# Performance work log

Measured on AMD Instinct MI355X. Metric: run time of the kernel, lower is better.

## Reference

```python
import jax, jax.numpy as jnp
import numpy as np


def _normal_distance(n1, n2):
    # Cosine-style normal distance: 1 - <n1, n2>. The original module stubs
    # this as 0; we use the canonical mesh-normal loss so the cdist+argmin+
    # gather chain is exercised end-to-end.
    return 1.0 - jnp.sum(n1 * n2, axis=-1)


def setup_inputs() -> dict:
    key = jax.random.key(0)
    k1, k2, k3, k4 = jax.random.split(key, 4)
    N, M = 8192, 32768
    pred_pts = jax.random.normal(k1, (1, N, 3), dtype=jnp.float32)
    pred_nrm = jax.random.normal(k2, (1, N, 3), dtype=jnp.float32)
    gt_pts = jax.random.normal(k3, (1, M, 3), dtype=jnp.float32)
    gt_nrm = jax.random.normal(k4, (1, M, 3), dtype=jnp.float32)
    # unit normals, as on a real mesh
    pred_nrm = pred_nrm / jnp.linalg.norm(pred_nrm, axis=-1, keepdims=True)
    gt_nrm = gt_nrm / jnp.linalg.norm(gt_nrm, axis=-1, keepdims=True)
    return {
        "predicted_points_batch": pred_pts,
        "predicted_normals_batch": pred_nrm,
        "gt_points_batch": gt_pts,
        "gt_normals_batch": gt_nrm,
    }


def reference(predicted_points_batch, predicted_normals_batch,
              gt_points_batch, gt_normals_batch):
    # Original forward returns inside the first loop iteration -> element 0 only.
    p = predicted_points_batch[0]    # [N,3]
    pn = predicted_normals_batch[0]  # [N,3]
    g = gt_points_batch[0]           # [M,3]
    gn = gt_normals_batch[0]         # [M,3]

    # Squared pairwise distances (monotone in true cdist; only argmin is used).
    # d2[i,j] = |p_i|^2 + |g_j|^2 - 2 p_i . g_j   -> one [N,M] intermediate.
    d2 = (jnp.sum(p * p, axis=1)[:, None]
          + jnp.sum(g * g, axis=1)[None, :]
          - 2.0 * (p @ g.T))                      # [N,M]

    gt_idx = jnp.argmin(d2, axis=1)    # nearest gt point per predicted point, [N]
    pr_idx = jnp.argmin(d2, axis=0)    # nearest predicted point per gt point, [M]

    nearest_gt_normals = gn[gt_idx]    # [N,3]
    nearest_pr_normals = pn[pr_idx]    # [M,3]

    dist1 = _normal_distance(pn, nearest_gt_normals)  # [N]
    dist2 = _normal_distance(gn, nearest_pr_normals)  # [M]
    return jnp.mean(dist1) + jnp.mean(dist2)
```

## Files before the change

### kernel.cpp

```cpp
#include <hip/hip_runtime.h>
#include <stdint.h>
#include <float.h>

#define BLK 256
#define IPT 8
#define OWNERS (BLK * IPT)
#define SLICE 128
#define SUB 64

typedef unsigned long long ull;

__device__ __forceinline__ unsigned int ford(float f) {
    int b = __float_as_int(f);
    return (b >= 0) ? ((unsigned)b ^ 0x80000000u) : ~(unsigned)b;
}
__device__ __forceinline__ float ford_inv(unsigned int u) {
    int b = (u & 0x80000000u) ? (int)(u ^ 0x80000000u) : (int)~u;
    return __int_as_float(b);
}

__global__ __launch_bounds__(BLK) void nn_min_dual(
    const float* __restrict__ p, const float* __restrict__ g,
    ull* __restrict__ rowmin, ull* __restrict__ colmin,
    int rowBlocks, int rowSlices, int colSlices)
{
    __shared__ float4 sb[SLICE];

    const float* A; const float* B; ull* outmin; int id, nSlices;
    if ((int)blockIdx.x < rowBlocks) {
        id = blockIdx.x;             A = p; B = g; outmin = rowmin; nSlices = rowSlices;
    } else {
        id = blockIdx.x - rowBlocks; A = g; B = p; outmin = colmin; nSlices = colSlices;
    }
    const int chunk = id / nSlices;
    const int slice = id - chunk * nSlices;
    const int s0 = slice * SLICE;

    if (threadIdx.x < SLICE) {
        int s = s0 + threadIdx.x;
        float bx = B[3 * s], by = B[3 * s + 1], bz = B[3 * s + 2];
        float w = fmaf(bz, bz, fmaf(by, by, bx * bx));
        sb[threadIdx.x] = make_float4(bx, by, bz, w);
    }

    const int o0 = chunk * OWNERS + threadIdx.x;
    float ax[IPT], ay[IPT], az[IPT], best[IPT];
    int base[IPT];
#pragma unroll
    for (int r = 0; r < IPT; ++r) {
        int o = o0 + r * BLK;
        ax[r] = -2.0f * A[3 * o];
        ay[r] = -2.0f * A[3 * o + 1];
        az[r] = -2.0f * A[3 * o + 2];
        best[r] = FLT_MAX;
        base[r] = s0;
    }
    __syncthreads();

    for (int st = 0; st < SLICE; st += SUB) {
        float prev[IPT];
#pragma unroll
        for (int r = 0; r < IPT; ++r) prev[r] = best[r];
#pragma unroll 4
        for (int k = st; k < st + SUB; ++k) {
            float4 q = sb[k];
#pragma unroll
            for (int r = 0; r < IPT; ++r) {
                float v = fmaf(ax[r], q.x, fmaf(ay[r], q.y, fmaf(az[r], q.z, q.w)));
                best[r] = fminf(best[r], v);
            }
        }
#pragma unroll
        for (int r = 0; r < IPT; ++r)
            if (best[r] < prev[r]) base[r] = s0 + st;
    }

#pragma unroll
    for (int r = 0; r < IPT; ++r) {
        ull packed = ((ull)ford(best[r]) << 32) | (unsigned)base[r];
        atomicMin(&outmin[o0 + r * BLK], packed);
    }
}

__global__ __launch_bounds__(BLK) void finalize_kernel(
    const ull* __restrict__ rowmin, const ull* __restrict__ colmin,
    const float* __restrict__ p, const float* __restrict__ g,
    const float* __restrict__ pn, const float* __restrict__ gn,
    float* __restrict__ out, int N, int M, float invN, float invM)
{
    int t = blockIdx.x * BLK + threadIdx.x;
    float c = 0.0f;
    if (t < N + M) {
        const float* A; const float* B; const float* An; const float* Bn;
        ull packed; int o; float inv;
        if (t < N) { o = t;     A = p; B = g; An = pn; Bn = gn; packed = rowmin[o]; inv = invN; }
        else       { o = t - N; A = g; B = p; An = gn; Bn = pn; packed = colmin[o]; inv = invM; }

        float ax = -2.0f * A[3 * o];
        float ay = -2.0f * A[3 * o + 1];
        float az = -2.0f * A[3 * o + 2];
        float bestf = ford_inv((unsigned int)(packed >> 32));
        int base = (int)(packed & 0xffffffffull);

        int idx = base;
        for (int j = 0; j < SUB; ++j) {
            int s = base + j;
            float bx = B[3 * s], by = B[3 * s + 1], bz = B[3 * s + 2];
            float w = fmaf(bz, bz, fmaf(by, by, bx * bx));
            float v = fmaf(ax, bx, fmaf(ay, by, fmaf(az, bz, w)));
            if (v == bestf) { idx = s; break; }
        }

        float d = An[3 * o] * Bn[3 * idx] + An[3 * o + 1] * Bn[3 * idx + 1]
                + An[3 * o + 2] * Bn[3 * idx + 2];
        c = (1.0f - d) * inv;
    }
#pragma unroll
    for (int off = 32; off > 0; off >>= 1) c += __shfl_down(c, off, 64);
    __shared__ float partial[BLK / 64];
    if ((threadIdx.x & 63) == 0) partial[threadIdx.x >> 6] = c;
    __syncthreads();
    if (threadIdx.x == 0) {
        float s = 0.0f;
#pragma unroll
        for (int w = 0; w < BLK / 64; ++w) s += partial[w];
        atomicAdd(out, s);
    }
}

extern "C" void kernel_launch(void* const* d_in, const int* in_sizes, int n_in,
                              void* d_out, int out_size, void* d_ws, size_t ws_size,
                              hipStream_t stream) {
    const float* p  = (const float*)d_in[0];
    const float* pn = (const float*)d_in[1];
    const float* g  = (const float*)d_in[2];
    const float* gn = (const float*)d_in[3];
    const int N = in_sizes[0] / 3;
    const int M = in_sizes[2] / 3;

    ull* rowmin = (ull*)d_ws;
    ull* colmin = rowmin + N;
    float* out = (float*)d_out;

    hipMemsetAsync(d_ws, 0xFF, (size_t)(N + M) * sizeof(ull), stream);
    hipMemsetAsync(d_out, 0, sizeof(float), stream);

    const int rowSlices = M / SLICE;
    const int colSlices = N / SLICE;
    const int rowBlocks = (N / OWNERS) * rowSlices;
    const int colBlocks = (M / OWNERS) * colSlices;
    nn_min_dual<<<rowBlocks + colBlocks, BLK, 0, stream>>>(
        p, g, rowmin, colmin, rowBlocks, rowSlices, colSlices);

    int tot = N + M;
    finalize_kernel<<<(tot + BLK - 1) / BLK, BLK, 0, stream>>>(
        rowmin, colmin, p, g, pn, gn, out, N, M, 1.0f / N, 1.0f / M);
}
```

Measured before the change: 114.4 us.

## Pack distance FMAs into float2 vectors and simplify finalize reduction

The main distance loop now stores the slice in SoA shared arrays and computes two candidates at once with packed float2 FMAs (v_pk_fma_f32), which is meant to halve the FMA instruction count in the hot loop. The finalize kernel moves to 64-thread blocks with a single-wavefront reduction, its search loop no longer breaks early (it keeps the first exact match), and the output-zeroing memset is folded into the first kernel. Extra fminf operations per pair and the loss of the early exit in finalize may offset part of the gain.

```diff
diff --git a/kernel.cpp b/kernel.cpp
--- a/kernel.cpp
+++ b/kernel.cpp
@@ -7,8 +7,14 @@
 #define OWNERS (BLK * IPT)
 #define SLICE 128
 #define SUB 64
+#define FBLK 64
 
 typedef unsigned long long ull;
+typedef float v2f __attribute__((ext_vector_type(2)));
+
+__device__ __forceinline__ v2f fma2(v2f a, v2f b, v2f c) {
+    return __builtin_elementwise_fma(a, b, c);
+}
 
 __device__ __forceinline__ unsigned int ford(float f) {
     int b = __float_as_int(f);
@@ -22,9 +28,11 @@
 __global__ __launch_bounds__(BLK) void nn_min_dual(
     const float* __restrict__ p, const float* __restrict__ g,
     ull* __restrict__ rowmin, ull* __restrict__ colmin,
-    int rowBlocks, int rowSlices, int colSlices)
+    float* __restrict__ out, int rowBlocks, int rowSlices, int colSlices)
 {
-    __shared__ float4 sb[SLICE];
+    __shared__ float sbx[SLICE], sby[SLICE], sbz[SLICE], sbw[SLICE];
+
+    if (blockIdx.x == 0 && threadIdx.x == 0) *out = 0.0f;
 
     const float* A; const float* B; ull* outmin; int id, nSlices;
     if ((int)blockIdx.x < rowBlocks) {
@@ -40,18 +48,23 @@
         int s = s0 + threadIdx.x;
         float bx = B[3 * s], by = B[3 * s + 1], bz = B[3 * s + 2];
         float w = fmaf(bz, bz, fmaf(by, by, bx * bx));
-        sb[threadIdx.x] = make_float4(bx, by, bz, w);
+        sbx[threadIdx.x] = bx; sby[threadIdx.x] = by;
+        sbz[threadIdx.x] = bz; sbw[threadIdx.x] = w;
     }
 
     const int o0 = chunk * OWNERS + threadIdx.x;
-    float ax[IPT], ay[IPT], az[IPT], best[IPT];
+    v2f ax2[IPT], ay2[IPT], az2[IPT];
+    float best[IPT];
     int base[IPT];
 #pragma unroll
     for (int r = 0; r < IPT; ++r) {
         int o = o0 + r * BLK;
-        ax[r] = -2.0f * A[3 * o];
-        ay[r] = -2.0f * A[3 * o + 1];
-        az[r] = -2.0f * A[3 * o + 2];
+        float axv = -2.0f * A[3 * o];
+        float ayv = -2.0f * A[3 * o + 1];
+        float azv = -2.0f * A[3 * o + 2];
+        ax2[r] = (v2f){axv, axv};
+        ay2[r] = (v2f){ayv, ayv};
+        az2[r] = (v2f){azv, azv};
         best[r] = FLT_MAX;
         base[r] = s0;
     }
@@ -61,13 +74,18 @@
         float prev[IPT];
 #pragma unroll
         for (int r = 0; r < IPT; ++r) prev[r] = best[r];
-#pragma unroll 4
-        for (int k = st; k < st + SUB; ++k) {
-            float4 q = sb[k];
+#pragma unroll 2
+        for (int k = st; k < st + SUB; k += 2) {
+            v2f qx = *(const v2f*)&sbx[k];
+            v2f qy = *(const v2f*)&sby[k];
+            v2f qz = *(const v2f*)&sbz[k];
+            v2f qw = *(const v2f*)&sbw[k];
 #pragma unroll
             for (int r = 0; r < IPT; ++r) {
-                float v = fmaf(ax[r], q.x, fmaf(ay[r], q.y, fmaf(az[r], q.z, q.w)));
-                best[r] = fminf(best[r], v);
+                v2f t = fma2(az2[r], qz, qw);
+                t = fma2(ay2[r], qy, t);
+                t = fma2(ax2[r], qx, t);
+                best[r] = fminf(fminf(t.x, t.y), best[r]);
             }
         }
 #pragma unroll
@@ -82,13 +100,13 @@
     }
 }
 
-__global__ __launch_bounds__(BLK) void finalize_kernel(
+__global__ __launch_bounds__(FBLK) void finalize_kernel(
     const ull* __restrict__ rowmin, const ull* __restrict__ colmin,
     const float* __restrict__ p, const float* __restrict__ g,
     const float* __restrict__ pn, const float* __restrict__ gn,
     float* __restrict__ out, int N, int M, float invN, float invM)
 {
-    int t = blockIdx.x * BLK + threadIdx.x;
+    int t = blockIdx.x * FBLK + threadIdx.x;
     float c = 0.0f;
     if (t < N + M) {
         const float* A; const float* B; const float* An; const float* Bn;
@@ -100,16 +118,19 @@
         float ay = -2.0f * A[3 * o + 1];
         float az = -2.0f * A[3 * o + 2];
         float bestf = ford_inv((unsigned int)(packed >> 32));
-        int base = (int)(packed & 0xffffffffull);
+        int b0 = (int)(packed & 0xffffffffull);
 
-        int idx = base;
-        for (int j = 0; j < SUB; ++j) {
-            int s = base + j;
+        int idx = 0x7fffffff;
+#pragma unroll 4
+        for (int jj = 0; jj < SUB; ++jj) {
+            int s = b0 + jj;
             float bx = B[3 * s], by = B[3 * s + 1], bz = B[3 * s + 2];
             float w = fmaf(bz, bz, fmaf(by, by, bx * bx));
             float v = fmaf(ax, bx, fmaf(ay, by, fmaf(az, bz, w)));
-            if (v == bestf) { idx = s; break; }
+            int cand = (v == bestf) ? s : 0x7fffffff;
+            idx = (cand < idx) ? cand : idx;
         }
+        if (idx == 0x7fffffff) idx = b0;
 
         float d = An[3 * o] * Bn[3 * idx] + An[3 * o + 1] * Bn[3 * idx + 1]
                 + An[3 * o + 2] * Bn[3 * idx + 2];
@@ -117,15 +138,7 @@
     }
 #pragma unroll
     for (int off = 32; off > 0; off >>= 1) c += __shfl_down(c, off, 64);
-    __shared__ float partial[BLK / 64];
-    if ((threadIdx.x & 63) == 0) partial[threadIdx.x >> 6] = c;
-    __syncthreads();
-    if (threadIdx.x == 0) {
-        float s = 0.0f;
-#pragma unroll
-        for (int w = 0; w < BLK / 64; ++w) s += partial[w];
-        atomicAdd(out, s);
-    }
+    if (threadIdx.x == 0) atomicAdd(out, c);
 }
 
 extern "C" void kernel_launch(void* const* d_in, const int* in_sizes, int n_in,
@@ -137,22 +150,21 @@
     const float* gn = (const float*)d_in[3];
     const int N = in_sizes[0] / 3;
     const int M = in_sizes[2] / 3;
+    float* out = (float*)d_out;
 
     ull* rowmin = (ull*)d_ws;
     ull* colmin = rowmin + N;
-    float* out = (float*)d_out;
 
     hipMemsetAsync(d_ws, 0xFF, (size_t)(N + M) * sizeof(ull), stream);
-    hipMemsetAsync(d_out, 0, sizeof(float), stream);
 
     const int rowSlices = M / SLICE;
     const int colSlices = N / SLICE;
     const int rowBlocks = (N / OWNERS) * rowSlices;
     const int colBlocks = (M / OWNERS) * colSlices;
     nn_min_dual<<<rowBlocks + colBlocks, BLK, 0, stream>>>(
-        p, g, rowmin, colmin, rowBlocks, rowSlices, colSlices);
+        p, g, rowmin, colmin, out, rowBlocks, rowSlices, colSlices);
 
-    int tot = N + M;
-    finalize_kernel<<<(tot + BLK - 1) / BLK, BLK, 0, stream>>>(
+    const int tot = N + M;
+    finalize_kernel<<<(tot + FBLK - 1) / FBLK, FBLK, 0, stream>>>(
         rowmin, colmin, p, g, pn, gn, out, N, M, 1.0f / N, 1.0f / M);
 }
```

Result: no change. 116.0 us (+1.4%).
